# Kernel tuning notes

Measured on AMD Instinct MI355X. Metric: run time of the kernel, lower is better.

The kernel has to match this reference:

```python
import jax, jax.numpy as jnp
import numpy as np

EPS = 1e-10


def setup_inputs() -> dict:
    key = jax.random.key(0)
    k_in, k_len, k_u, k_w, k_b, k_cb = jax.random.split(key, 6)
    B, S, D_in = 16, 4096, 512
    G, C, D_out = 2, 320, 256
    inputs = jax.random.normal(k_in, (B, S, D_in), dtype=jnp.float32)
    valid_lengths = jax.random.randint(k_len, (B,), 1, S + 1, dtype=jnp.int64)
    noise_u = jax.random.uniform(k_u, (B, S, G, C), dtype=jnp.float32)
    # projector params (nn.Linear default init scale is irrelevant for correctness)
    W = jax.random.normal(k_w, (G * C, D_in), dtype=jnp.float32) * (1.0 / np.sqrt(D_in))
    b = jax.random.normal(k_b, (G * C,), dtype=jnp.float32) * 0.01
    codebook = jax.random.uniform(k_cb, (G, C, D_out // G), dtype=jnp.float32,
                                  minval=-1.0 / C, maxval=1.0 / C)
    temperature = jnp.asarray(2.0, dtype=jnp.float32)
    return {"inputs": inputs, "valid_lengths": valid_lengths, "noise_u": noise_u,
            "W": W, "b": b, "codebook": codebook, "temperature": temperature}


def reference(inputs, valid_lengths, noise_u, W, b, codebook, temperature):
    B, S, _ = inputs.shape
    G, C, Dg = codebook.shape
    # dense projector GEMM: [B,S,Din] @ [Din,G*C]
    logits = (jnp.einsum('bsi,oi->bso', inputs, W) + b).reshape(B, S, G, C)
    # gumbel-softmax with straight-through hard selection (F.gumbel_softmax)
    gumbels = -jnp.log(-jnp.log(noise_u + EPS) + EPS)
    y_soft = jax.nn.softmax((logits + gumbels) / temperature, axis=-1)
    idx = jnp.argmax(y_soft, axis=-1)                       # [B,S,G]
    y_hard = jax.nn.one_hot(idx, C, dtype=y_soft.dtype)
    choice_probs = y_hard - jax.lax.stop_gradient(y_soft) + y_soft
    # masked usage stats over valid positions
    soft_probs = jax.nn.softmax(logits, axis=-1)            # [B,S,G,C]
    mask = (jnp.arange(S)[None, :] < valid_lengths[:, None]).astype(soft_probs.dtype)
    masked_sum = jnp.einsum('bsgc,bs->gc', soft_probs, mask)
    usage = masked_sum / jnp.sum(mask)
    # per-group codebook lookup via einsum against small table
    quantized = jnp.einsum('bsgc,gcd->bsgd', choice_probs, codebook).reshape(B, S, G * Dg)
    return quantized, usage
```

## Files before the change

kernel.cpp:

```cpp
#include <hip/hip_runtime.h>
#include <math.h>

#define NB 16
#define NS 4096
#define DIN 512
#define NG 2
#define NC 320
#define GC 640
#define DG 128
#define NROW (NB*NS)
#define EPSV 1e-10f

typedef __attribute__((ext_vector_type(4))) float f32x4;
typedef __attribute__((ext_vector_type(8))) _Float16 f16x8;
typedef __attribute__((ext_vector_type(4))) _Float16 f16x4v;

__device__ __forceinline__ void gload_lds16(const void* g, void* l) {
    __builtin_amdgcn_global_load_lds(
        (const __attribute__((address_space(1))) void*)g,
        (__attribute__((address_space(3))) void*)l,
        16, 0, 0);
}

__global__ __launch_bounds__(256) void cvt_split(
    const float* __restrict__ src, _Float16* __restrict__ h,
    _Float16* __restrict__ l, int n4)
{
    int i = blockIdx.x * 256 + threadIdx.x;
    if (i >= n4) return;
    float4 v = ((const float4*)src)[i];
    f16x4v vh, vl;
    float xs[4] = {v.x, v.y, v.z, v.w};
    #pragma unroll
    for (int j = 0; j < 4; ++j) {
        _Float16 hh = (_Float16)xs[j];
        vh[j] = hh;
        vl[j] = (_Float16)((xs[j] - (float)hh) * 2048.0f);
    }
    ((f16x4v*)h)[i] = vh;
    ((f16x4v*)l)[i] = vl;
}

__global__ __launch_bounds__(512, 3) void mfma_logits2(
    const float* __restrict__ X,
    const _Float16* __restrict__ Wh, const _Float16* __restrict__ Wl,
    const float* __restrict__ bias, float* __restrict__ logits)
{
    __shared__ _Float16 sA[2][2][128 * 32];
    __shared__ _Float16 sB[2][2][128 * 32];

    const int t = threadIdx.x;
    const int lane = t & 63;
    const int w = t >> 6;
    const int wm = w >> 2, wn = w & 3;

    const int p = blockIdx.x;
    const int o = (p & 7) * 320 + (p >> 3);
    const int mb = o / 5, nb = o - mb * 5;
    const int row0 = mb * 128, n0 = nb * 128;

    const int rl = lane >> 2;
    const int sl = (lane & 3) ^ ((lane >> 3) & 3);

    auto stageB = [&](int b, int k0) {
        int ro = 16 * w + rl;
        size_t gb = (size_t)(n0 + ro) * DIN + k0 + 8 * sl;
        gload_lds16(Wh + gb, &sB[b][0][w * 512]);
        gload_lds16(Wl + gb, &sB[b][1][w * 512]);
    };

    const int ar = t >> 2, aq = t & 3;
    const int aidx = ar * 32 + 8 * (aq ^ ((ar >> 1) & 3));
    const float* aga = X + (size_t)(row0 + ar) * DIN + 8 * aq;

    float4 a0, a1;
    auto loadA = [&](int k0) {
        a0 = ((const float4*)(aga + k0))[0];
        a1 = ((const float4*)(aga + k0))[1];
    };
    auto writeA = [&](int b) {
        float xs[8] = {a0.x, a0.y, a0.z, a0.w, a1.x, a1.y, a1.z, a1.w};
        f16x8 h, l;
        #pragma unroll
        for (int j = 0; j < 8; ++j) {
            _Float16 hh = (_Float16)xs[j];
            h[j] = hh;
            l[j] = (_Float16)((xs[j] - (float)hh) * 2048.0f);
        }
        *(f16x8*)&sA[b][0][aidx] = h;
        *(f16x8*)&sA[b][1][aidx] = l;
    };

    f32x4 accA[4][2], accB[4][2];
    const f32x4 zz = {0.f, 0.f, 0.f, 0.f};
    #pragma unroll
    for (int mt = 0; mt < 4; ++mt)
        #pragma unroll
        for (int nt = 0; nt < 2; ++nt) { accA[mt][nt] = zz; accB[mt][nt] = zz; }

    loadA(0);
    stageB(0, 0);
    writeA(0);
    __syncthreads();

    for (int ks = 0; ks < 16; ++ks) {
        const int cur = ks & 1;
        if (ks < 15) { loadA((ks + 1) * 32); stageB(cur ^ 1, (ks + 1) * 32); }

        f16x8 ah[4], al[4], bh[2], bl[2];
        #pragma unroll
        for (int mt = 0; mt < 4; ++mt) {
            int r = wm * 64 + mt * 16 + (lane & 15);
            int idx = r * 32 + 8 * ((lane >> 4) ^ ((r >> 1) & 3));
            ah[mt] = *(const f16x8*)&sA[cur][0][idx];
            al[mt] = *(const f16x8*)&sA[cur][1][idx];
        }
        #pragma unroll
        for (int nt = 0; nt < 2; ++nt) {
            int r = wn * 32 + nt * 16 + (lane & 15);
            int idx = r * 32 + 8 * ((lane >> 4) ^ ((r >> 1) & 3));
            bh[nt] = *(const f16x8*)&sB[cur][0][idx];
            bl[nt] = *(const f16x8*)&sB[cur][1][idx];
        }
        #pragma unroll
        for (int mt = 0; mt < 4; ++mt)
            #pragma unroll
            for (int nt = 0; nt < 2; ++nt) {
                accA[mt][nt] = __builtin_amdgcn_mfma_f32_16x16x32_f16(ah[mt], bh[nt], accA[mt][nt], 0, 0, 0);
                accB[mt][nt] = __builtin_amdgcn_mfma_f32_16x16x32_f16(ah[mt], bl[nt], accB[mt][nt], 0, 0, 0);
                accB[mt][nt] = __builtin_amdgcn_mfma_f32_16x16x32_f16(al[mt], bh[nt], accB[mt][nt], 0, 0, 0);
            }

        if (ks < 15) writeA(cur ^ 1);
        __syncthreads();
    }

    #pragma unroll
    for (int nt = 0; nt < 2; ++nt) {
        int col = n0 + wn * 32 + nt * 16 + (lane & 15);
        float bv = bias[col];
        #pragma unroll
        for (int mt = 0; mt < 4; ++mt) {
            #pragma unroll
            for (int q = 0; q < 4; ++q) {
                int row = row0 + wm * 64 + mt * 16 + (lane >> 4) * 4 + q;
                logits[(size_t)row * GC + col] =
                    accA[mt][nt][q] + accB[mt][nt][q] * (1.0f / 2048.0f) + bv;
            }
        }
    }
}

#define RTB 32
__global__ __launch_bounds__(256, 8) void epilogue(
    const float* __restrict__ logits, const int* __restrict__ vlen,
    const float* __restrict__ U, const float* __restrict__ CB,
    float* __restrict__ out, float* __restrict__ gacc)
{
    __shared__ float uacc[GC];
    const int t = threadIdx.x;
    const int lane = t & 63;
    const int wid = t >> 6;
    const int row0 = blockIdx.x * RTB;

    for (int i = t; i < GC; i += 256) uacc[i] = 0.0f;
    __syncthreads();

    const int vl = vlen[row0 >> 12];

    float ureg[10];
    #pragma unroll
    for (int j = 0; j < 10; ++j) ureg[j] = 0.0f;

    #pragma unroll
    for (int r = 0; r < 8; ++r) {
        const int row = row0 + wid * 8 + r;
        const bool valid = (row & (NS - 1)) < vl;

        float lg[10], zz[10];
        #pragma unroll
        for (int j = 0; j < 10; ++j)
            lg[j] = logits[(size_t)row * GC + lane + 64 * j];
        #pragma unroll
        for (int j = 0; j < 10; ++j) {
            float u = U[(size_t)row * GC + lane + 64 * j];
            zz[j] = lg[j] - logf(-logf(u + EPSV) + EPSV);
        }

        #pragma unroll
        for (int g = 0; g < 2; ++g) {
            const int j0 = g * 5;

            float mv = zz[j0];
            #pragma unroll
            for (int j = j0 + 1; j < j0 + 5; ++j) mv = fmaxf(mv, zz[j]);
            #pragma unroll
            for (int d = 1; d < 64; d <<= 1) mv = fmaxf(mv, __shfl_xor(mv, d));

            int c = 0;
            #pragma unroll
            for (int jj = 4; jj >= 0; --jj) {
                unsigned long long b = __ballot(zz[j0 + jj] == mv);
                if (b) c = (__ffsll(b) - 1) + 64 * jj;
            }

            float pe[5], s2 = 0.0f;
            #pragma unroll
            for (int jj = 0; jj < 5; ++jj) {
                pe[jj] = __expf(lg[j0 + jj]);
                s2 += pe[jj];
            }
            #pragma unroll
            for (int d = 1; d < 64; d <<= 1) s2 += __shfl_xor(s2, d);
            if (valid) {
                const float inv = 1.0f / s2;
                #pragma unroll
                for (int jj = 0; jj < 5; ++jj) ureg[j0 + jj] += pe[jj] * inv;
            }

            const float2 cv = ((const float2*)(CB + ((size_t)g * NC + c) * DG))[lane];
            ((float2*)(out + (size_t)row * (NG * DG) + g * DG))[lane] = cv;
        }
    }

    #pragma unroll
    for (int j = 0; j < 10; ++j)
        atomicAdd(&uacc[lane + 64 * j], ureg[j]);

    __syncthreads();
    for (int i = t; i < GC; i += 256) atomicAdd(&gacc[i], uacc[i]);
}

__global__ void finalize_usage(const float* __restrict__ gacc,
                               const int* __restrict__ vlen,
                               float* __restrict__ usage_out)
{
    int total = 0;
    #pragma unroll
    for (int b = 0; b < NB; ++b) total += vlen[b];
    int o = threadIdx.x;
    if (o < GC) usage_out[o] = gacc[o] / (float)total;
}

#define RT 32
#define KC 8
#define NIT (DIN/KC)

__global__ void transpose_w(const float* __restrict__ W, float* __restrict__ Wt) {
    int idx = blockIdx.x * 256 + threadIdx.x;
    if (idx >= GC * DIN) return;
    int k = idx / GC, o = idx - k * GC;
    Wt[idx] = W[(size_t)o * DIN + k];
}

__global__ __launch_bounds__(256, 2) void fused_main(
    const float* __restrict__ X, const int* __restrict__ vlen,
    const float* __restrict__ U, const float* __restrict__ Wt,
    const float* __restrict__ bias, const float* __restrict__ CB,
    const float* __restrict__ tptr, float* __restrict__ out,
    float* __restrict__ gacc)
{
    __shared__ __align__(16) float WtC[2][KC][GC];
    __shared__ __align__(16) float AC[2][RT][KC];
    __shared__ float uacc[GC];

    const int t = threadIdx.x;
    const int lane = t & 63;
    const int wid = t >> 6;
    const int row0 = blockIdx.x * RT;

    for (int i = t; i < GC; i += 256) uacc[i] = 0.0f;

    float acc[8][10];
    #pragma unroll
    for (int r = 0; r < 8; ++r)
        #pragma unroll
        for (int j = 0; j < 10; ++j) acc[r][j] = 0.0f;

    auto stage = [&](int b, int k0) {
        const float* gw = Wt + (size_t)k0 * GC;
        #pragma unroll
        for (int i = 0; i < 5; ++i) {
            int base = (wid * 5 + i) * 256;
            gload_lds16(gw + base + 4 * lane, &WtC[b][0][0] + base);
        }
        if (wid == 0) {
            const float* gx = X + (size_t)(row0 + (lane >> 1)) * DIN + k0 + 4 * (lane & 1);
            gload_lds16(gx, &AC[b][0][0]);
        }
    };

    stage(0, 0);
    __syncthreads();

    int cur = 0;
    for (int it = 0; it < NIT; ++it) {
        if (it + 1 < NIT) stage(cur ^ 1, (it + 1) * KC);
        #pragma unroll
        for (int kk = 0; kk < KC; ++kk) {
            float w[10];
            #pragma unroll
            for (int j = 0; j < 10; ++j) w[j] = WtC[cur][kk][lane + 64 * j];
            #pragma unroll
            for (int r = 0; r < 8; ++r) {
                float a = AC[cur][wid * 8 + r][kk];
                #pragma unroll
                for (int j = 0; j < 10; ++j) acc[r][j] = fmaf(a, w[j], acc[r][j]);
            }
        }
        __syncthreads();
        cur ^= 1;
    }

    float bv[10];
    #pragma unroll
    for (int j = 0; j < 10; ++j) bv[j] = bias[lane + 64 * j];
    #pragma unroll
    for (int r = 0; r < 8; ++r)
        #pragma unroll
        for (int j = 0; j < 10; ++j) acc[r][j] += bv[j];

    const float T = *tptr;
    const int vl = vlen[row0 >> 12];

    #pragma unroll
    for (int r = 0; r < 8; ++r) {
        const int row = row0 + wid * 8 + r;
        const int ss = row & (NS - 1);
        const bool valid = ss < vl;

        float z[10];
        #pragma unroll
        for (int j = 0; j < 10; ++j) {
            float u = U[(size_t)row * GC + lane + 64 * j];
            float gn = -logf(-logf(u + EPSV) + EPSV);
            z[j] = (acc[r][j] + gn) / T;
        }

        #pragma unroll
        for (int g = 0; g < 2; ++g) {
            const int j0 = g * 5;
            float mv = z[j0];
            int mo = lane + 64 * j0;
            #pragma unroll
            for (int j = j0 + 1; j < j0 + 5; ++j) {
                if (z[j] > mv) { mv = z[j]; mo = lane + 64 * j; }
            }
            #pragma unroll
            for (int d = 1; d < 64; d <<= 1) {
                float ov = __shfl_xor(mv, d);
                int   oo = __shfl_xor(mo, d);
                if (ov > mv || (ov == mv && oo < mo)) { mv = ov; mo = oo; }
            }
            float se = 0.0f;
            #pragma unroll
            for (int j = j0; j < j0 + 5; ++j) se += expf(z[j] - mv);
            #pragma unroll
            for (int d = 1; d < 64; d <<= 1) se += __shfl_xor(se, d);
            float y = 1.0f / se;
            float q = (1.0f - y) + y;

            float m2 = acc[r][j0];
            #pragma unroll
            for (int j = j0 + 1; j < j0 + 5; ++j) m2 = fmaxf(m2, acc[r][j]);
            #pragma unroll
            for (int d = 1; d < 64; d <<= 1) m2 = fmaxf(m2, __shfl_xor(m2, d));
            float pe[5];
            float s2 = 0.0f;
            #pragma unroll
            for (int jj = 0; jj < 5; ++jj) {
                pe[jj] = expf(acc[r][j0 + jj] - m2);
                s2 += pe[jj];
            }
            #pragma unroll
            for (int d = 1; d < 64; d <<= 1) s2 += __shfl_xor(s2, d);
            if (valid) {
                #pragma unroll
                for (int jj = 0; jj < 5; ++jj)
                    atomicAdd(&uacc[lane + 64 * (j0 + jj)], pe[jj] / s2);
            }

            const int c = mo - g * NC;
            const float2 cv = ((const float2*)(CB + ((size_t)g * NC + c) * DG))[lane];
            float2 ov2;
            ov2.x = q * cv.x;
            ov2.y = q * cv.y;
            ((float2*)(out + (size_t)row * (NG * DG) + g * DG))[lane] = ov2;
        }
    }

    __syncthreads();
    for (int i = t; i < GC; i += 256) atomicAdd(&gacc[i], uacc[i]);
}

extern "C" void kernel_launch(void* const* d_in, const int* in_sizes, int n_in,
                              void* d_out, int out_size, void* d_ws, size_t ws_size,
                              hipStream_t stream)
{
    const float* X    = (const float*)d_in[0];
    const int*   vlen = (const int*)d_in[1];
    const float* U    = (const float*)d_in[2];
    const float* W    = (const float*)d_in[3];
    const float* bias = (const float*)d_in[4];
    const float* CB   = (const float*)d_in[5];
    const float* T    = (const float*)d_in[6];
    float* out = (float*)d_out;

    char* ws = (char*)d_ws;
    float*     gacc = (float*)ws;
    _Float16*  Whh  = (_Float16*)(ws + 4096);
    _Float16*  Wll  = (_Float16*)(ws + 659456);
    float*     lgts = (float*)(ws + 1314816);
    float*     Wt   = (float*)(ws + 4096);
    const size_t need = 1314816ull + 167772160ull;

    hipMemsetAsync(gacc, 0, GC * sizeof(float), stream);

    if (ws_size >= need) {
        const int nw4 = GC * DIN / 4;
        cvt_split<<<(nw4 + 255) / 256, 256, 0, stream>>>(W, Whh, Wll, nw4);
        mfma_logits2<<<(NROW / 128) * 5, 512, 0, stream>>>(X, Whh, Wll, bias, lgts);
        epilogue<<<NROW / RTB, 256, 0, stream>>>(lgts, vlen, U, CB, out, gacc);
    } else {
        transpose_w<<<(GC * DIN + 255) / 256, 256, 0, stream>>>(W, Wt);
        fused_main<<<NROW / RT, 256, 0, stream>>>(X, vlen, U, Wt, bias, CB, T, out, gacc);
    }
    finalize_usage<<<1, GC, 0, stream>>>(gacc, vlen, out + (size_t)NROW * (NG * DG));
}
```

Baseline: 269.0 us.

## Prepack W into MFMA fragment layout and read B operand directly from global

The weight conversion kernel now writes the fp16 hi/lo split of W in a layout that matches the MFMA B-fragment order per k-slice and column tile. The GEMM then loads B fragments straight from global/L2 into registers, which drops the LDS staging buffers for B. Halving LDS use allows raising the occupancy hint from 3 to 4 blocks per CU, and the barrier is replaced by an explicit lgkmcnt wait plus s_barrier that is skipped on the last iteration. The risk is that B global loads are no longer prefetched a stage ahead, so their latency may be exposed inside the MFMA loop.

```diff
diff --git a/kernel.cpp b/kernel.cpp
--- a/kernel.cpp
+++ b/kernel.cpp
@@ -9,11 +9,12 @@
 #define GC 640
 #define DG 128
 #define NROW (NB*NS)
+#define NKT 16
+#define NCT 40
 #define EPSV 1e-10f
 
 typedef __attribute__((ext_vector_type(4))) float f32x4;
 typedef __attribute__((ext_vector_type(8))) _Float16 f16x8;
-typedef __attribute__((ext_vector_type(4))) _Float16 f16x4v;
 
 __device__ __forceinline__ void gload_lds16(const void* g, void* l) {
     __builtin_amdgcn_global_load_lds(
@@ -22,32 +23,34 @@
         16, 0, 0);
 }
 
-__global__ __launch_bounds__(256) void cvt_split(
-    const float* __restrict__ src, _Float16* __restrict__ h,
-    _Float16* __restrict__ l, int n4)
-{
-    int i = blockIdx.x * 256 + threadIdx.x;
-    if (i >= n4) return;
-    float4 v = ((const float4*)src)[i];
-    f16x4v vh, vl;
-    float xs[4] = {v.x, v.y, v.z, v.w};
-    #pragma unroll
-    for (int j = 0; j < 4; ++j) {
-        _Float16 hh = (_Float16)xs[j];
-        vh[j] = hh;
-        vl[j] = (_Float16)((xs[j] - (float)hh) * 2048.0f);
-    }
-    ((f16x4v*)h)[i] = vh;
-    ((f16x4v*)l)[i] = vl;
-}
-
-__global__ __launch_bounds__(512, 3) void mfma_logits2(
+__global__ __launch_bounds__(256) void cvt_split_pack(
+    const float* __restrict__ W, _Float16* __restrict__ hp, _Float16* __restrict__ lp)
+{
+    int idx = blockIdx.x * 256 + threadIdx.x;
+    if (idx >= GC * (DIN / 8)) return;
+    int col = idx >> 6, k8 = idx & 63;
+    int kslice = k8 >> 2, kq = k8 & 3, ntile = col >> 4;
+    int ln = (col & 15) + 16 * kq;
+    size_t dst = (((size_t)kslice * NCT + ntile) * 64 + ln) * 8;
+    const float* src = W + (size_t)col * DIN + k8 * 8;
+    f16x8 h, l;
+    #pragma unroll
+    for (int j = 0; j < 8; ++j) {
+        float x = src[j];
+        _Float16 hh = (_Float16)x;
+        h[j] = hh;
+        l[j] = (_Float16)((x - (float)hh) * 2048.0f);
+    }
+    *(f16x8*)(hp + dst) = h;
+    *(f16x8*)(lp + dst) = l;
+}
+
+__global__ __launch_bounds__(512, 4) void mfma_logits3(
     const float* __restrict__ X,
-    const _Float16* __restrict__ Wh, const _Float16* __restrict__ Wl,
+    const _Float16* __restrict__ Whp, const _Float16* __restrict__ Wlp,
     const float* __restrict__ bias, float* __restrict__ logits)
 {
     __shared__ _Float16 sA[2][2][128 * 32];
-    __shared__ _Float16 sB[2][2][128 * 32];
 
     const int t = threadIdx.x;
     const int lane = t & 63;
@@ -58,16 +61,7 @@
     const int o = (p & 7) * 320 + (p >> 3);
     const int mb = o / 5, nb = o - mb * 5;
     const int row0 = mb * 128, n0 = nb * 128;
-
-    const int rl = lane >> 2;
-    const int sl = (lane & 3) ^ ((lane >> 3) & 3);
-
-    auto stageB = [&](int b, int k0) {
-        int ro = 16 * w + rl;
-        size_t gb = (size_t)(n0 + ro) * DIN + k0 + 8 * sl;
-        gload_lds16(Wh + gb, &sB[b][0][w * 512]);
-        gload_lds16(Wl + gb, &sB[b][1][w * 512]);
-    };
+    const int ct0 = (n0 >> 4) + wn * 2;
 
     const int ar = t >> 2, aq = t & 3;
     const int aidx = ar * 32 + 8 * (aq ^ ((ar >> 1) & 3));
@@ -99,15 +93,23 @@
         for (int nt = 0; nt < 2; ++nt) { accA[mt][nt] = zz; accB[mt][nt] = zz; }
 
     loadA(0);
-    stageB(0, 0);
     writeA(0);
-    __syncthreads();
-
-    for (int ks = 0; ks < 16; ++ks) {
+    asm volatile("s_waitcnt lgkmcnt(0)" ::: "memory");
+    __builtin_amdgcn_s_barrier();
+    __builtin_amdgcn_sched_barrier(0);
+
+    for (int ks = 0; ks < NKT; ++ks) {
         const int cur = ks & 1;
-        if (ks < 15) { loadA((ks + 1) * 32); stageB(cur ^ 1, (ks + 1) * 32); }
-
-        f16x8 ah[4], al[4], bh[2], bl[2];
+        if (ks < NKT - 1) loadA((ks + 1) * 32);
+
+        f16x8 bh[2], bl[2];
+        #pragma unroll
+        for (int nt = 0; nt < 2; ++nt) {
+            size_t off = (((size_t)ks * NCT) + ct0 + nt) * 64 + lane;
+            bh[nt] = *(const f16x8*)(Whp + off * 8);
+            bl[nt] = *(const f16x8*)(Wlp + off * 8);
+        }
+        f16x8 ah[4], al[4];
         #pragma unroll
         for (int mt = 0; mt < 4; ++mt) {
             int r = wm * 64 + mt * 16 + (lane & 15);
@@ -116,13 +118,6 @@
             al[mt] = *(const f16x8*)&sA[cur][1][idx];
         }
         #pragma unroll
-        for (int nt = 0; nt < 2; ++nt) {
-            int r = wn * 32 + nt * 16 + (lane & 15);
-            int idx = r * 32 + 8 * ((lane >> 4) ^ ((r >> 1) & 3));
-            bh[nt] = *(const f16x8*)&sB[cur][0][idx];
-            bl[nt] = *(const f16x8*)&sB[cur][1][idx];
-        }
-        #pragma unroll
         for (int mt = 0; mt < 4; ++mt)
             #pragma unroll
             for (int nt = 0; nt < 2; ++nt) {
@@ -131,8 +126,12 @@
                 accB[mt][nt] = __builtin_amdgcn_mfma_f32_16x16x32_f16(al[mt], bh[nt], accB[mt][nt], 0, 0, 0);
             }
 
-        if (ks < 15) writeA(cur ^ 1);
-        __syncthreads();
+        if (ks < NKT - 1) {
+            writeA(cur ^ 1);
+            asm volatile("s_waitcnt lgkmcnt(0)" ::: "memory");
+            __builtin_amdgcn_s_barrier();
+            __builtin_amdgcn_sched_barrier(0);
+        }
     }
 
     #pragma unroll
@@ -408,8 +407,8 @@
 
     char* ws = (char*)d_ws;
     float*     gacc = (float*)ws;
-    _Float16*  Whh  = (_Float16*)(ws + 4096);
-    _Float16*  Wll  = (_Float16*)(ws + 659456);
+    _Float16*  Whp  = (_Float16*)(ws + 4096);
+    _Float16*  Wlp  = (_Float16*)(ws + 659456);
     float*     lgts = (float*)(ws + 1314816);
     float*     Wt   = (float*)(ws + 4096);
     const size_t need = 1314816ull + 167772160ull;
@@ -417,9 +416,8 @@
     hipMemsetAsync(gacc, 0, GC * sizeof(float), stream);
 
     if (ws_size >= need) {
-        const int nw4 = GC * DIN / 4;
-        cvt_split<<<(nw4 + 255) / 256, 256, 0, stream>>>(W, Whh, Wll, nw4);
-        mfma_logits2<<<(NROW / 128) * 5, 512, 0, stream>>>(X, Whh, Wll, bias, lgts);
+        cvt_split_pack<<<(GC * (DIN / 8) + 255) / 256, 256, 0, stream>>>(W, Whp, Wlp);
+        mfma_logits3<<<(NROW / 128) * 5, 512, 0, stream>>>(X, Whp, Wlp, bias, lgts);
         epilogue<<<NROW / RTB, 256, 0, stream>>>(lgts, vlen, U, CB, out, gacc);
     } else {
         transpose_w<<<(GC * DIN + 255) / 256, 256, 0, stream>>>(W, Wt);
```

Result: no change. 272.3 us (+1.2%).
